# Kernel tuning notes

Measured on AMD Instinct MI355X. Metric: run time of the kernel, lower is better.

## Reference

```python
import jax, jax.numpy as jnp
import numpy as np

B, N, D = 128, 196, 1024          # batch, num image features, d_model == hidden_dim
E = 1024                           # embed_dim
V = 10000                          # vocab_size
NH = 8                             # num_heads
T = 20                             # max caption length
DH = D // NH


def setup_inputs() -> dict:
    key = jax.random.key(0)
    ks = jax.random.split(key, 16)
    u = lambda k, shape, s=0.1: jax.random.uniform(k, shape, jnp.float32, -s, s)
    lengths = jnp.sort(jax.random.randint(ks[1], (B,), 1, T + 1))[::-1]
    lengths = lengths.at[0].set(T)  # ensure max(lengths) == T
    return {
        "enc_features": jax.random.normal(ks[0], (B, N, D), jnp.float32),
        "captions": jax.random.randint(ks[2], (B, T), 0, V),
        "lengths": lengths,
        "embed_W": u(ks[3], (V, E)),
        # LSTMCell params (PyTorch layout: gates ordered i,f,g,o)
        "W_ih": u(ks[4], (4 * D, E + D), 0.03),
        "b_ih": u(ks[5], (4 * D,), 0.03),
        "W_hh": u(ks[6], (4 * D, D), 0.03),
        "b_hh": u(ks[7], (4 * D,), 0.03),
        # AoA block
        "Wq": u(ks[8], (D, D), 0.03), "bq": jnp.zeros((D,), jnp.float32),
        "Wk": u(ks[9], (D, D), 0.03), "bk": jnp.zeros((D,), jnp.float32),
        "Wv": u(ks[10], (D, D), 0.03), "bv": jnp.zeros((D,), jnp.float32),
        "W_aoa": u(ks[11], (2 * D, 2 * D), 0.02), "b_aoa": jnp.zeros((2 * D,), jnp.float32),
        # weight-normed predict layer (dim=0): W = g * v / ||v||_row
        "pred_v": u(ks[12], (V, D)),
        "pred_g": jnp.ones((V,), jnp.float32),
        "pred_b": jnp.zeros((V,), jnp.float32),
    }


def reference(enc_features, captions, lengths, embed_W, W_ih, b_ih, W_hh, b_hh,
              Wq, bq, Wk, bk, Wv, bv, W_aoa, b_aoa, pred_v, pred_g, pred_b):
    # eval mode: dropouts are identity; ss_prob == 0.
    scale = 1.0 / jnp.sqrt(jnp.asarray(DH, jnp.float32))
    mean_f = jnp.mean(enc_features, axis=1)                      # [B, D]
    # K/V projections of enc_features are step-invariant: hoist out of the loop.
    K = (enc_features @ Wk.T + bk).reshape(B, N, NH, DH).transpose(0, 2, 1, 3)  # [B,NH,N,DH]
    Vv = (enc_features @ Wv.T + bv).reshape(B, N, NH, DH).transpose(0, 2, 1, 3)
    # weight-norm predict matrix (dim=0 row-wise norm)
    Wn = pred_g[:, None] * pred_v / jnp.linalg.norm(pred_v, axis=1, keepdims=True)  # [V, D]

    active = (jnp.arange(T)[:, None] < lengths[None, :])         # [T, B]
    toks = captions.T                                            # [T, B]

    def step(carry, inp):
        h, m, ctx = carry
        it, act = inp
        emb = embed_W[it]                                        # [B, E]
        x = jnp.concatenate([emb, mean_f + ctx], axis=-1)        # [B, E+D]
        gates = x @ W_ih.T + b_ih + h @ W_hh.T + b_hh            # [B, 4D]
        i, f, g, o = jnp.split(gates, 4, axis=-1)
        m2 = jax.nn.sigmoid(f) * m + jax.nn.sigmoid(i) * jnp.tanh(g)
        h2 = jax.nn.sigmoid(o) * jnp.tanh(m2)                    # [B, D]
        # single-query multi-head attention
        q = (h2 @ Wq.T + bq).reshape(B, NH, DH)                  # [B, NH, DH]
        scores = jnp.einsum('bhd,bhnd->bhn', q, K) * scale       # [B, NH, N]
        p = jax.nn.softmax(scores, axis=-1)
        att = jnp.einsum('bhn,bhnd->bhd', p, Vv).reshape(B, D)   # [B, D]
        # AoA: Linear(2D->2D) + GLU on cat(att, query)
        a = jnp.concatenate([att, h2], axis=-1) @ W_aoa.T + b_aoa
        a1, a2 = jnp.split(a, 2, axis=-1)
        ctx2 = a1 * jax.nn.sigmoid(a2)                           # [B, D]
        preds = ctx2 @ Wn.T + pred_b                             # [B, V]
        preds = jnp.where(act[:, None], preds, 0.0)
        return (h2, m2, ctx2), preds

    z = jnp.zeros((B, D), jnp.float32)
    _, preds = jax.lax.scan(step, (z, z, z), (toks, active))     # [T, B, V]
    return preds.transpose(1, 0, 2)                              # [B, T, V], zero-padded
```

## Files before the change

### kernel.cpp

```cpp
#include <hip/hip_runtime.h>
#include <hip/hip_bf16.h>
#include <cstdint>

#define BB 128
#define TT 20
#define VV 10000
#define DD 1024
#define NHH 8
#define DHH 128
#define NN 196

typedef float f32x4 __attribute__((ext_vector_type(4)));
typedef __bf16 bf16x8 __attribute__((ext_vector_type(8)));
typedef unsigned int u32x4 __attribute__((ext_vector_type(4)));
typedef unsigned int u32x2 __attribute__((ext_vector_type(2)));

__device__ __forceinline__ unsigned short f2bf(float x) {
  unsigned u = __float_as_uint(x);
  u += 0x7FFFu + ((u >> 16) & 1u);
  return (unsigned short)(u >> 16);
}
__device__ __forceinline__ float bf2f(unsigned short h) {
  return __uint_as_float(((unsigned)h) << 16);
}
__device__ __forceinline__ float sigm(float x) { return 1.f / (1.f + __expf(-x)); }
__device__ __forceinline__ unsigned pk2(float lo, float hi) {
  return (unsigned)f2bf(lo) | ((unsigned)f2bf(hi) << 16);
}
__device__ __forceinline__ int xcd_swz(int orig, int nb) {
  int q = nb >> 3, r = nb & 7;
  int x = orig & 7, i = orig >> 3;
  return (x < r ? x * (q + 1) : r * (q + 1) + (x - r) * q) + i;
}
__device__ __forceinline__ void gl16(const void* g, void* l) {
  __builtin_amdgcn_global_load_lds((const __attribute__((address_space(1))) void*)g,
                                   (__attribute__((address_space(3))) void*)l, 16, 0, 0);
}

template<int N> __device__ __forceinline__ void waitvm() {
  if constexpr (N == 0)       asm volatile("s_waitcnt vmcnt(0)" ::: "memory");
  else if constexpr (N == 3)  asm volatile("s_waitcnt vmcnt(3)" ::: "memory");
  else if constexpr (N == 5)  asm volatile("s_waitcnt vmcnt(5)" ::: "memory");
  else if constexpr (N == 6)  asm volatile("s_waitcnt vmcnt(6)" ::: "memory");
  else if constexpr (N == 8)  asm volatile("s_waitcnt vmcnt(8)" ::: "memory");
  else if constexpr (N == 10) asm volatile("s_waitcnt vmcnt(10)" ::: "memory");
  else if constexpr (N == 12) asm volatile("s_waitcnt vmcnt(12)" ::: "memory");
  else if constexpr (N == 16) asm volatile("s_waitcnt vmcnt(16)" ::: "memory");
}
#define LGKM0()  asm volatile("s_waitcnt lgkmcnt(0)" ::: "memory")
#define SCHED0() __builtin_amdgcn_sched_barrier(0)

template<int BM, int BN, int MODE, int DEP, bool RF>
__launch_bounds__(256)
__global__ void gemmp(const unsigned short* __restrict__ A, int lda,
                      const unsigned short* __restrict__ W, int ldw,
                      int nkt, int N, int ncol,
                      const float* __restrict__ bias,
                      float* __restrict__ outF, unsigned short* __restrict__ outB,
                      float* __restrict__ mbuf, const float* __restrict__ meanf,
                      unsigned short* __restrict__ xaoa, unsigned short* __restrict__ xn2,
                      const int* __restrict__ lengths)
{
  constexpr int SZA = BM * 128;
  constexpr int SZB = BN * 128;
  constexpr int NJ = BN / 16;
  constexpr int MI = BM / 64;
  constexpr int S = BM / 32 + BN / 32;
  __shared__ char smem[DEP * (SZA + SZB)];

  const int nb = gridDim.x;
  const int wg = xcd_swz(blockIdx.x, nb);
  int xi, rowt;
  if (RF) { const int nrow = nb / ncol; rowt = wg % nrow; xi = wg / nrow; }
  else    { xi = wg % ncol; rowt = wg / ncol; }
  const int colbase = xi * BN;
  const int rowbase = rowt * BM;
  const int tid = threadIdx.x;
  const int lane = tid & 63, wv = tid >> 6;
  const int wrow = wv * (BM / 4);
  const int lr = lane & 15;
  const int srow = lane >> 3;
  const int schunk = ((lane & 7) ^ srow) * 8;

  auto stage = [&](int t, int buf) {
    char* sA = smem + buf * (SZA + SZB);
    char* sB = sA + SZA;
    const int k0 = t << 6;
    #pragma unroll
    for (int s = 0; s < BM / 32; ++s) {
      const int rb = s * 32 + wv * 8;
      gl16(A + (size_t)(rowbase + rb + srow) * lda + k0 + schunk, sA + rb * 128);
    }
    #pragma unroll
    for (int s = 0; s < BN / 32; ++s) {
      const int rb = s * 32 + wv * 8;
      int br = colbase + rb + srow;
      if (MODE == 2) br = br < N ? br : N - 1;
      gl16(W + (size_t)br * ldw + k0 + schunk, sB + rb * 128);
    }
  };

  f32x4 acc[MI][NJ];
  const f32x4 zero = {0.f, 0.f, 0.f, 0.f};
  #pragma unroll
  for (int i = 0; i < MI; ++i)
    #pragma unroll
    for (int j = 0; j < NJ; ++j) acc[i][j] = zero;

  #pragma unroll
  for (int t = 0; t < DEP; ++t) stage(t, t);

  const int axor = (lr & 7) << 4;
  const int ccol = (lane >> 4) * 16;
  int buf = 0;
  for (int i = 0; i < nkt; ++i) {
    const int rem = nkt - 1 - i;
    if (rem >= DEP - 1)            waitvm<S * (DEP - 1)>();
    else if (DEP > 2 && rem == 1)  waitvm<S>();
    else                           waitvm<0>();
    __builtin_amdgcn_s_barrier();
    SCHED0();
    const char* sA = smem + buf * (SZA + SZB);
    const char* sB = sA + SZA;
    bf16x8 af[MI][2], bfr[NJ][2];
    #pragma unroll
    for (int ii = 0; ii < MI; ++ii)
      #pragma unroll
      for (int kk = 0; kk < 2; ++kk)
        af[ii][kk] = *reinterpret_cast<const bf16x8*>(
            sA + (wrow + ii * 16 + lr) * 128 + ((kk * 64 + ccol) ^ axor));
    #pragma unroll
    for (int j = 0; j < NJ; ++j)
      #pragma unroll
      for (int kk = 0; kk < 2; ++kk)
        bfr[j][kk] = *reinterpret_cast<const bf16x8*>(
            sB + (j * 16 + lr) * 128 + ((kk * 64 + ccol) ^ axor));
    LGKM0();
    SCHED0();
    __builtin_amdgcn_s_barrier();
    SCHED0();
    if (i + DEP < nkt) stage(i + DEP, buf);
    #pragma unroll
    for (int kk = 0; kk < 2; ++kk)
      #pragma unroll
      for (int ii = 0; ii < MI; ++ii)
        #pragma unroll
        for (int j = 0; j < NJ; ++j)
          acc[ii][j] = __builtin_amdgcn_mfma_f32_16x16x32_bf16(af[ii][kk], bfr[j][kk], acc[ii][j], 0, 0, 0);
    buf = (buf == DEP - 1) ? 0 : buf + 1;
  }

  const int rg4 = (lane >> 4) * 4;

  if constexpr (MODE == 0) {
    #pragma unroll
    for (int ii = 0; ii < MI; ++ii)
      #pragma unroll
      for (int j = 0; j < NJ; ++j) {
        const int gcol = colbase + j * 16 + lr;
        #pragma unroll
        for (int r = 0; r < 4; ++r)
          outF[(size_t)(rowbase + wrow + ii * 16 + rg4 + r) * N + gcol] = acc[ii][j][r];
      }
  } else if constexpr (MODE == 1) {
    #pragma unroll
    for (int ii = 0; ii < MI; ++ii)
      #pragma unroll
      for (int j = 0; j < NJ; ++j) {
        const int gcol = colbase + j * 16 + lr;
        const float bv = bias[gcol];
        #pragma unroll
        for (int r = 0; r < 4; ++r)
          outB[(size_t)(rowbase + wrow + ii * 16 + rg4 + r) * N + gcol] = f2bf(acc[ii][j][r] + bv);
      }
  } else if constexpr (MODE == 2) {
    #pragma unroll
    for (int ii = 0; ii < MI; ++ii)
      #pragma unroll
      for (int j = 0; j < NJ; ++j) {
        const int gcol = colbase + j * 16 + lr;
        if (gcol >= N) continue;
        const float bv = bias[gcol];
        #pragma unroll
        for (int r = 0; r < 4; ++r) {
          const int gr = rowbase + wrow + ii * 16 + rg4 + r;
          const int tt = gr >> 7, bb = gr & 127;
          outF[((size_t)bb * TT + tt) * VV + gcol] =
              (tt < lengths[bb]) ? acc[ii][j][r] + bv : 0.f;
        }
      }
  } else if constexpr (MODE == 3) {
    const float b0 = bias[colbase + lr], b1 = bias[colbase + 16 + lr];
    float a0[MI][4], a1[MI][4];
    #pragma unroll
    for (int ii = 0; ii < MI; ++ii)
      #pragma unroll
      for (int r = 0; r < 4; ++r) {
        const int grow = rowbase + wrow + ii * 16 + rg4 + r;
        a0[ii][r] = acc[ii][0][r] + b0 + outF[(size_t)grow * 4096 + colbase + lr];
        a1[ii][r] = acc[ii][1][r] + b1 + outF[(size_t)grow * 4096 + colbase + 16 + lr];
      }
    const int d = (colbase >> 2) + (lr & 7);
    #pragma unroll
    for (int ii = 0; ii < MI; ++ii)
      #pragma unroll
      for (int r = 0; r < 4; ++r) {
        const float fg = __shfl_xor(a0[ii][r], 8);
        const float og = __shfl_xor(a1[ii][r], 8);
        if (lr < 8) {
          const int grow = rowbase + wrow + ii * 16 + rg4 + r;
          const float m2 = sigm(fg) * mbuf[(size_t)grow * DD + d] + sigm(a0[ii][r]) * tanhf(a1[ii][r]);
          const float h2 = sigm(og) * tanhf(m2);
          mbuf[(size_t)grow * DD + d] = m2;
          const unsigned short hb = f2bf(h2);
          xaoa[(size_t)grow * 2048 + 1024 + d] = hb;
          xn2[(size_t)grow * 2048 + 1024 + d] = hb;
        }
      }
  } else {
    const int d = (colbase >> 1) + lr;
    const float b0 = bias[colbase + lr], b1 = bias[colbase + 16 + lr];
    #pragma unroll
    for (int ii = 0; ii < MI; ++ii)
      #pragma unroll
      for (int r = 0; r < 4; ++r) {
        const int grow = rowbase + wrow + ii * 16 + rg4 + r;
        const float av1 = acc[ii][0][r] + b0;
        const float av2 = acc[ii][1][r] + b1;
        const float c2 = av1 * sigm(av2);
        outB[(size_t)grow * DD + d] = f2bf(c2);
        xn2[(size_t)grow * 2048 + d] = f2bf(meanf[(size_t)grow * DD + d] + c2);
      }
  }
}

__launch_bounds__(256)
__global__ void attn_kernel(const float* __restrict__ qbuf, const float* __restrict__ bq,
                            const unsigned short* __restrict__ KV, unsigned short* __restrict__ xaoa) {
  const int bh = blockIdx.x, b = bh >> 3, h = bh & 7;
  const int tid = threadIdx.x;
  const int lane = tid & 63, wv = tid >> 6;
  __shared__ float qs[DHH];
  __shared__ float sc[NN + 4];
  __shared__ float pvred[2][DHH];
  __shared__ float redm[4], reds[4];
  if (tid < DHH)
    qs[tid] = bq[h * DHH + tid] + qbuf[(size_t)b * DD + h * DHH + tid];
  __syncthreads();
  if (tid < NN) {
    const unsigned short* kr = KV + ((size_t)(b * NN + tid)) * 2048 + h * DHH;
    float a = 0.f;
    #pragma unroll
    for (int j = 0; j < 16; ++j) {
      u32x4 kk = *reinterpret_cast<const u32x4*>(kr + j * 8);
      #pragma unroll
      for (int w = 0; w < 4; ++w) {
        a += bf2f((unsigned short)(kk[w] & 0xffffu)) * qs[j * 8 + w * 2]
           + bf2f((unsigned short)(kk[w] >> 16)) * qs[j * 8 + w * 2 + 1];
      }
    }
    sc[tid] = a * 0.08838834764831845f;
  }
  __syncthreads();
  float v = (tid < NN) ? sc[tid] : -1e30f;
  #pragma unroll
  for (int o = 32; o; o >>= 1) v = fmaxf(v, __shfl_xor(v, o));
  if (lane == 0) redm[wv] = v;
  __syncthreads();
  const float mx = fmaxf(fmaxf(redm[0], redm[1]), fmaxf(redm[2], redm[3]));
  float e = 0.f;
  if (tid < NN) { e = __expf(sc[tid] - mx); sc[tid] = e; }
  float s = e;
  #pragma unroll
  for (int o = 32; o; o >>= 1) s += __shfl_xor(s, o);
  if (lane == 0) reds[wv] = s;
  __syncthreads();
  const float inv = 1.f / (reds[0] + reds[1] + reds[2] + reds[3]);
  const int d = tid & 127, half = tid >> 7;
  const unsigned short* vr = KV + ((size_t)(b * NN + half * 98)) * 2048 + 1024 + h * DHH + d;
  float a = 0.f;
  for (int n = 0; n < 98; ++n) a += sc[half * 98 + n] * bf2f(vr[(size_t)n * 2048]);
  pvred[half][d] = a;
  __syncthreads();
  if (tid < DHH)
    xaoa[(size_t)b * 2048 + h * DHH + tid] = f2bf((pvred[0][tid] + pvred[1][tid]) * inv);
}

__launch_bounds__(256)
__global__ void meanconv_kernel(const float* __restrict__ enc, float* __restrict__ meanf,
                                unsigned short* __restrict__ encb) {
  int b = blockIdx.x >> 2, d = (blockIdx.x & 3) * 256 + threadIdx.x;
  const float* p = enc + (size_t)b * NN * DD + d;
  unsigned short* q = encb + (size_t)b * NN * DD + d;
  float s = 0.f;
  for (int n = 0; n < NN; ++n) {
    float x = p[(size_t)n * DD];
    s += x;
    q[(size_t)n * DD] = f2bf(x);
  }
  meanf[(size_t)b * DD + d] = s * (1.0f / (float)NN);
}

__launch_bounds__(256)
__global__ void conv4_kernel(const float* __restrict__ src, unsigned short* __restrict__ dst) {
  int i = blockIdx.x * 256 + threadIdx.x;
  f32x4 v = *reinterpret_cast<const f32x4*>(src + (size_t)i * 4);
  u32x2 o = { pk2(v[0], v[1]), pk2(v[2], v[3]) };
  *reinterpret_cast<u32x2*>(dst + (size_t)i * 4) = o;
}

__launch_bounds__(256)
__global__ void wcatI_kernel(const float* __restrict__ W_ih, const float* __restrict__ W_hh,
                             unsigned short* __restrict__ Wcat) {
  int i = blockIdx.x * 256 + threadIdx.x;
  int rp = i / 768, c4 = (i - rp * 768) * 4;
  int rem = rp & 31, g = rem >> 3, d = (rp >> 5) * 8 + (rem & 7);
  int orig = g * 1024 + d;
  const float* src = (c4 < 2048) ? (W_ih + (size_t)orig * 2048 + c4)
                                 : (W_hh + (size_t)orig * 1024 + (c4 - 2048));
  f32x4 v = *reinterpret_cast<const f32x4*>(src);
  u32x2 o = { pk2(v[0], v[1]), pk2(v[2], v[3]) };
  *reinterpret_cast<u32x2*>(Wcat + (size_t)rp * 3072 + c4) = o;
}

__launch_bounds__(256)
__global__ void waoaI_kernel(const float* __restrict__ W_aoa, unsigned short* __restrict__ Wo) {
  int i = blockIdx.x * 256 + threadIdx.x;
  int rp = i >> 9, c4 = (i & 511) * 4;
  int rem = rp & 31, half = rem >> 4, d = (rp >> 5) * 16 + (rem & 15);
  int orig = half * 1024 + d;
  f32x4 v = *reinterpret_cast<const f32x4*>(W_aoa + (size_t)orig * 2048 + c4);
  u32x2 o = { pk2(v[0], v[1]), pk2(v[2], v[3]) };
  *reinterpret_cast<u32x2*>(Wo + (size_t)rp * 2048 + c4) = o;
}

__launch_bounds__(256)
__global__ void kvw4_kernel(const float* __restrict__ Wk, const float* __restrict__ Wv,
                            unsigned short* __restrict__ Wkv) {
  int i = blockIdx.x * 256 + threadIdx.x;
  int row = i >> 8, c4 = (i & 255) << 2;
  const float* src = (row < 1024) ? (Wk + (size_t)row * 1024 + c4)
                                  : (Wv + (size_t)(row - 1024) * 1024 + c4);
  f32x4 v = *reinterpret_cast<const f32x4*>(src);
  u32x2 o = { pk2(v[0], v[1]), pk2(v[2], v[3]) };
  *reinterpret_cast<u32x2*>(Wkv + (size_t)row * 1024 + c4) = o;
}

__launch_bounds__(256)
__global__ void bias_kernel(const float* __restrict__ b_ih, const float* __restrict__ b_hh,
                            const float* __restrict__ b_aoa, const float* __restrict__ bk,
                            const float* __restrict__ bv, float* __restrict__ bcombI,
                            float* __restrict__ baoaI, float* __restrict__ bkv) {
  int i = blockIdx.x * 256 + threadIdx.x;
  {
    int rem = i & 31, g = rem >> 3, d = (i >> 5) * 8 + (rem & 7);
    int orig = g * 1024 + d;
    bcombI[i] = b_ih[orig] + b_hh[orig];
  }
  if (i < 2048) {
    int rem = i & 31, half = rem >> 4, d = (i >> 5) * 16 + (rem & 15);
    baoaI[i] = b_aoa[half * 1024 + d];
    bkv[i] = (i < 1024) ? bk[i] : bv[i - 1024];
  }
}

__launch_bounds__(256)
__global__ void init_kernel(const float* __restrict__ meanf, float* __restrict__ m,
                            unsigned short* __restrict__ x2_0) {
  int idx = blockIdx.x * 256 + threadIdx.x;
  int b = idx >> 10, d = idx & 1023;
  m[idx] = 0.f;
  x2_0[(size_t)b * 2048 + d] = f2bf(meanf[idx]);
  x2_0[(size_t)b * 2048 + 1024 + d] = 0;
}

__launch_bounds__(256)
__global__ void wn_kernel(const float* __restrict__ pred_v, const float* __restrict__ pred_g,
                          unsigned short* __restrict__ Wn) {
  int v = blockIdx.x, tid = threadIdx.x;
  f32x4 x = *reinterpret_cast<const f32x4*>(pred_v + (size_t)v * DD + tid * 4);
  float s = x[0] * x[0] + x[1] * x[1] + x[2] * x[2] + x[3] * x[3];
  #pragma unroll
  for (int o = 32; o; o >>= 1) s += __shfl_down(s, o);
  __shared__ float red[4];
  if ((tid & 63) == 0) red[tid >> 6] = s;
  __syncthreads();
  float inv = pred_g[v] * rsqrtf(red[0] + red[1] + red[2] + red[3]);
  u32x2 o = { pk2(x[0] * inv, x[1] * inv), pk2(x[2] * inv, x[3] * inv) };
  *reinterpret_cast<u32x2*>(Wn + (size_t)v * DD + tid * 4) = o;
}

__launch_bounds__(256)
__global__ void emb4_kernel(const float* __restrict__ embed_W, const int* __restrict__ captions,
                            unsigned short* __restrict__ embAll) {
  int i = blockIdx.x * 256 + threadIdx.x;
  int j4 = (i & 255) << 2, b = (i >> 8) & 127, t = i >> 15;
  int tok = captions[b * TT + t];
  f32x4 v = *reinterpret_cast<const f32x4*>(embed_W + (size_t)tok * DD + j4);
  u32x2 o = { pk2(v[0], v[1]), pk2(v[2], v[3]) };
  *reinterpret_cast<u32x2*>(embAll + ((size_t)t * BB + b) * DD + j4) = o;
}

extern "C" void kernel_launch(void* const* d_in, const int* in_sizes, int n_in,
                              void* d_out, int out_size, void* d_ws, size_t ws_size,
                              hipStream_t stream) {
  const float* enc      = (const float*)d_in[0];
  const int*   captions = (const int*)d_in[1];
  const int*   lengths  = (const int*)d_in[2];
  const float* embed_W  = (const float*)d_in[3];
  const float* W_ih     = (const float*)d_in[4];
  const float* b_ih     = (const float*)d_in[5];
  const float* W_hh     = (const float*)d_in[6];
  const float* b_hh     = (const float*)d_in[7];
  const float* Wq       = (const float*)d_in[8];
  const float* bq       = (const float*)d_in[9];
  const float* Wk       = (const float*)d_in[10];
  const float* bk       = (const float*)d_in[11];
  const float* Wv       = (const float*)d_in[12];
  const float* bv       = (const float*)d_in[13];
  const float* W_aoa    = (const float*)d_in[14];
  const float* b_aoa    = (const float*)d_in[15];
  const float* pred_v   = (const float*)d_in[16];
  const float* pred_g   = (const float*)d_in[17];
  const float* pred_b   = (const float*)d_in[18];
  float* out = (float*)d_out;

  char* base = (char*)d_ws;
  size_t off = 0;
  auto alloc = [&](size_t bytes) -> char* {
    char* p = base + off;
    off = (off + bytes + 255) & ~(size_t)255;
    return p;
  };
  unsigned short* KV     = (unsigned short*)alloc((size_t)BB * NN * 2048 * 2);
  unsigned short* WcatI  = (unsigned short*)alloc((size_t)4096 * 3072 * 2);
  unsigned short* WaoaI  = (unsigned short*)alloc((size_t)2048 * 2048 * 2);
  unsigned short* Wq_b   = (unsigned short*)alloc((size_t)DD * DD * 2);
  unsigned short* Wkv_b  = (unsigned short*)alloc((size_t)2048 * 1024 * 2);
  float* bcombI          = (float*)alloc(4096 * 4);
  float* baoaI           = (float*)alloc(2048 * 4);
  float* bkv             = (float*)alloc(2048 * 4);
  float* meanf           = (float*)alloc((size_t)BB * DD * 4);
  float* mbuf            = (float*)alloc((size_t)BB * DD * 4);
  unsigned short* embAll = (unsigned short*)alloc((size_t)TT * BB * DD * 2);
  unsigned short* x2     = (unsigned short*)alloc((size_t)2 * BB * 2048 * 2);
  char* uni = alloc((size_t)BB * NN * DD * 2);
  unsigned short* encb = (unsigned short*)uni;
  size_t ua = 0;
  auto carve = [&](size_t b) -> char* { char* p = uni + ua; ua = (ua + b + 255) & ~(size_t)255; return p; };
  float* Eall               = (float*)carve((size_t)TT * BB * 4096 * 4);
  unsigned short* predinAll = (unsigned short*)carve((size_t)TT * BB * DD * 2);
  unsigned short* xaoa      = (unsigned short*)carve((size_t)BB * 2048 * 2);
  float* qbuf               = (float*)carve((size_t)BB * DD * 4);
  unsigned short* Wn_b      = (unsigned short*)uni;
  if (off > ws_size || ua > (size_t)BB * NN * DD * 2) return;

  meanconv_kernel<<<512, 256, 0, stream>>>(enc, meanf, encb);
  wcatI_kernel<<<12288, 256, 0, stream>>>(W_ih, W_hh, WcatI);
  conv4_kernel<<<1024, 256, 0, stream>>>(Wq, Wq_b);
  waoaI_kernel<<<4096, 256, 0, stream>>>(W_aoa, WaoaI);
  kvw4_kernel<<<2048, 256, 0, stream>>>(Wk, Wv, Wkv_b);
  bias_kernel<<<16, 256, 0, stream>>>(b_ih, b_hh, b_aoa, bk, bv, bcombI, baoaI, bkv);
  emb4_kernel<<<2560, 256, 0, stream>>>(embed_W, captions, embAll);
  init_kernel<<<512, 256, 0, stream>>>(meanf, mbuf, x2);
  gemmp<128, 128, 1, 2, false><<<3136, 256, 0, stream>>>(encb, 1024, Wkv_b, 1024, 16, 2048, 16, bkv,
                                                         nullptr, KV, nullptr, nullptr, nullptr, nullptr, nullptr);
  gemmp<128, 128, 0, 2, true><<<640, 256, 0, stream>>>(embAll, 1024, WcatI, 3072, 16, 4096, 32, nullptr,
                                                       Eall, nullptr, nullptr, nullptr, nullptr, nullptr, nullptr);

  for (int t = 0; t < TT; ++t) {
    unsigned short* xc = x2 + (size_t)(t & 1) * BB * 2048;
    unsigned short* xn = x2 + (size_t)((t + 1) & 1) * BB * 2048;
    gemmp<64, 32, 3, 3, false><<<256, 256, 0, stream>>>(xc, 2048, WcatI + 1024, 3072, 32, 4096, 128, bcombI,
                                                        Eall + (size_t)t * BB * 4096, nullptr, mbuf, nullptr, xaoa, xn, nullptr);
    gemmp<64, 32, 0, 3, false><<<64, 256, 0, stream>>>(xaoa + 1024, 2048, Wq_b, 1024, 16, 1024, 32, nullptr,
                                                       qbuf, nullptr, nullptr, nullptr, nullptr, nullptr, nullptr);
    attn_kernel<<<BB * NHH, 256, 0, stream>>>(qbuf, bq, KV, xaoa);
    gemmp<64, 32, 4, 3, false><<<128, 256, 0, stream>>>(xaoa, 2048, WaoaI, 2048, 32, 2048, 64, baoaI,
                                                        nullptr, predinAll + (size_t)t * BB * DD, nullptr, meanf, nullptr, xn, nullptr);
  }

  wn_kernel<<<VV, 256, 0, stream>>>(pred_v, pred_g, Wn_b);
  gemmp<128, 128, 2, 2, true><<<1580, 256, 0, stream>>>(predinAll, 1024, Wn_b, 1024, 16, VV, 79, pred_b,
                                                        out, nullptr, nullptr, nullptr, nullptr, nullptr, lengths);
}
```

Measured before the change: 1.269 ms.

## Merge prep kernels into one launch, halve GEMM M-tile, split PV accumulators

Seven small preprocessing kernels (weight conversions, biases, embedding gather, init) are merged into one prep_kernel that dispatches on block index, removing per-launch overhead. The KV projection and final prediction GEMMs switch from 128x128 to 64x128 tiles with twice the grid, aiming for better CU occupancy and load balance. The attention PV loop uses two accumulators with partial unrolling to expose more memory-level parallelism. Smaller tiles reduce data reuse per block, and the block-index branching adds some divergence risk.

```diff
diff --git a/kernel.cpp b/kernel.cpp
--- a/kernel.cpp
+++ b/kernel.cpp
@@ -278,12 +278,93 @@
   const float inv = 1.f / (reds[0] + reds[1] + reds[2] + reds[3]);
   const int d = tid & 127, half = tid >> 7;
   const unsigned short* vr = KV + ((size_t)(b * NN + half * 98)) * 2048 + 1024 + h * DHH + d;
-  float a = 0.f;
-  for (int n = 0; n < 98; ++n) a += sc[half * 98 + n] * bf2f(vr[(size_t)n * 2048]);
-  pvred[half][d] = a;
+  const float* pr = sc + half * 98;
+  float a0 = 0.f, a1 = 0.f;
+  #pragma unroll 7
+  for (int n = 0; n < 98; n += 2) {
+    a0 += pr[n]     * bf2f(vr[(size_t)n * 2048]);
+    a1 += pr[n + 1] * bf2f(vr[(size_t)(n + 1) * 2048]);
+  }
+  pvred[half][d] = a0 + a1;
   __syncthreads();
   if (tid < DHH)
     xaoa[(size_t)b * 2048 + h * DHH + tid] = f2bf((pvred[0][tid] + pvred[1][tid]) * inv);
+}
+
+__launch_bounds__(256)
+__global__ void prep_kernel(const float* __restrict__ W_ih, const float* __restrict__ W_hh,
+                            const float* __restrict__ Wq, const float* __restrict__ W_aoa,
+                            const float* __restrict__ Wk, const float* __restrict__ Wv,
+                            const float* __restrict__ b_ih, const float* __restrict__ b_hh,
+                            const float* __restrict__ b_aoa, const float* __restrict__ bk,
+                            const float* __restrict__ bv,
+                            const float* __restrict__ embed_W, const int* __restrict__ captions,
+                            const float* __restrict__ meanf,
+                            unsigned short* __restrict__ WcatI, unsigned short* __restrict__ Wq_b,
+                            unsigned short* __restrict__ WaoaI, unsigned short* __restrict__ Wkv_b,
+                            float* __restrict__ bcombI, float* __restrict__ baoaI,
+                            float* __restrict__ bkv,
+                            unsigned short* __restrict__ embAll, float* __restrict__ mbuf,
+                            unsigned short* __restrict__ x2_0)
+{
+  const int bid = blockIdx.x, tid = threadIdx.x;
+  if (bid < 12288) {
+    int i = bid * 256 + tid;
+    int rp = i / 768, c4 = (i - rp * 768) * 4;
+    int rem = rp & 31, g = rem >> 3, d = (rp >> 5) * 8 + (rem & 7);
+    int orig = g * 1024 + d;
+    const float* src = (c4 < 2048) ? (W_ih + (size_t)orig * 2048 + c4)
+                                   : (W_hh + (size_t)orig * 1024 + (c4 - 2048));
+    f32x4 vv = *reinterpret_cast<const f32x4*>(src);
+    u32x2 o = { pk2(vv[0], vv[1]), pk2(vv[2], vv[3]) };
+    *reinterpret_cast<u32x2*>(WcatI + (size_t)rp * 3072 + c4) = o;
+  } else if (bid < 13312) {
+    int i = (bid - 12288) * 256 + tid;
+    f32x4 vv = *reinterpret_cast<const f32x4*>(Wq + (size_t)i * 4);
+    u32x2 o = { pk2(vv[0], vv[1]), pk2(vv[2], vv[3]) };
+    *reinterpret_cast<u32x2*>(Wq_b + (size_t)i * 4) = o;
+  } else if (bid < 17408) {
+    int i = (bid - 13312) * 256 + tid;
+    int rp = i >> 9, c4 = (i & 511) * 4;
+    int rem = rp & 31, half = rem >> 4, d = (rp >> 5) * 16 + (rem & 15);
+    int orig = half * 1024 + d;
+    f32x4 vv = *reinterpret_cast<const f32x4*>(W_aoa + (size_t)orig * 2048 + c4);
+    u32x2 o = { pk2(vv[0], vv[1]), pk2(vv[2], vv[3]) };
+    *reinterpret_cast<u32x2*>(WaoaI + (size_t)rp * 2048 + c4) = o;
+  } else if (bid < 19456) {
+    int i = (bid - 17408) * 256 + tid;
+    int row = i >> 8, c4 = (i & 255) << 2;
+    const float* src = (row < 1024) ? (Wk + (size_t)row * 1024 + c4)
+                                    : (Wv + (size_t)(row - 1024) * 1024 + c4);
+    f32x4 vv = *reinterpret_cast<const f32x4*>(src);
+    u32x2 o = { pk2(vv[0], vv[1]), pk2(vv[2], vv[3]) };
+    *reinterpret_cast<u32x2*>(Wkv_b + (size_t)row * 1024 + c4) = o;
+  } else if (bid < 19472) {
+    int i = (bid - 19456) * 256 + tid;
+    {
+      int rem = i & 31, g = rem >> 3, d = (i >> 5) * 8 + (rem & 7);
+      int orig = g * 1024 + d;
+      bcombI[i] = b_ih[orig] + b_hh[orig];
+    }
+    if (i < 2048) {
+      int rem = i & 31, half = rem >> 4, d = (i >> 5) * 16 + (rem & 15);
+      baoaI[i] = b_aoa[half * 1024 + d];
+      bkv[i] = (i < 1024) ? bk[i] : bv[i - 1024];
+    }
+  } else if (bid < 22032) {
+    int i = (bid - 19472) * 256 + tid;
+    int j4 = (i & 255) << 2, b = (i >> 8) & 127, t = i >> 15;
+    int tok = captions[b * TT + t];
+    f32x4 vv = *reinterpret_cast<const f32x4*>(embed_W + (size_t)tok * DD + j4);
+    u32x2 o = { pk2(vv[0], vv[1]), pk2(vv[2], vv[3]) };
+    *reinterpret_cast<u32x2*>(embAll + ((size_t)t * BB + b) * DD + j4) = o;
+  } else {
+    int idx = (bid - 22032) * 256 + tid;
+    int b = idx >> 10, d = idx & 1023;
+    mbuf[idx] = 0.f;
+    x2_0[(size_t)b * 2048 + d] = f2bf(meanf[idx]);
+    x2_0[(size_t)b * 2048 + 1024 + d] = 0;
+  }
 }
 
 __launch_bounds__(256)
@@ -302,79 +383,6 @@
 }
 
 __launch_bounds__(256)
-__global__ void conv4_kernel(const float* __restrict__ src, unsigned short* __restrict__ dst) {
-  int i = blockIdx.x * 256 + threadIdx.x;
-  f32x4 v = *reinterpret_cast<const f32x4*>(src + (size_t)i * 4);
-  u32x2 o = { pk2(v[0], v[1]), pk2(v[2], v[3]) };
-  *reinterpret_cast<u32x2*>(dst + (size_t)i * 4) = o;
-}
-
-__launch_bounds__(256)
-__global__ void wcatI_kernel(const float* __restrict__ W_ih, const float* __restrict__ W_hh,
-                             unsigned short* __restrict__ Wcat) {
-  int i = blockIdx.x * 256 + threadIdx.x;
-  int rp = i / 768, c4 = (i - rp * 768) * 4;
-  int rem = rp & 31, g = rem >> 3, d = (rp >> 5) * 8 + (rem & 7);
-  int orig = g * 1024 + d;
-  const float* src = (c4 < 2048) ? (W_ih + (size_t)orig * 2048 + c4)
-                                 : (W_hh + (size_t)orig * 1024 + (c4 - 2048));
-  f32x4 v = *reinterpret_cast<const f32x4*>(src);
-  u32x2 o = { pk2(v[0], v[1]), pk2(v[2], v[3]) };
-  *reinterpret_cast<u32x2*>(Wcat + (size_t)rp * 3072 + c4) = o;
-}
-
-__launch_bounds__(256)
-__global__ void waoaI_kernel(const float* __restrict__ W_aoa, unsigned short* __restrict__ Wo) {
-  int i = blockIdx.x * 256 + threadIdx.x;
-  int rp = i >> 9, c4 = (i & 511) * 4;
-  int rem = rp & 31, half = rem >> 4, d = (rp >> 5) * 16 + (rem & 15);
-  int orig = half * 1024 + d;
-  f32x4 v = *reinterpret_cast<const f32x4*>(W_aoa + (size_t)orig * 2048 + c4);
-  u32x2 o = { pk2(v[0], v[1]), pk2(v[2], v[3]) };
-  *reinterpret_cast<u32x2*>(Wo + (size_t)rp * 2048 + c4) = o;
-}
-
-__launch_bounds__(256)
-__global__ void kvw4_kernel(const float* __restrict__ Wk, const float* __restrict__ Wv,
-                            unsigned short* __restrict__ Wkv) {
-  int i = blockIdx.x * 256 + threadIdx.x;
-  int row = i >> 8, c4 = (i & 255) << 2;
-  const float* src = (row < 1024) ? (Wk + (size_t)row * 1024 + c4)
-                                  : (Wv + (size_t)(row - 1024) * 1024 + c4);
-  f32x4 v = *reinterpret_cast<const f32x4*>(src);
-  u32x2 o = { pk2(v[0], v[1]), pk2(v[2], v[3]) };
-  *reinterpret_cast<u32x2*>(Wkv + (size_t)row * 1024 + c4) = o;
-}
-
-__launch_bounds__(256)
-__global__ void bias_kernel(const float* __restrict__ b_ih, const float* __restrict__ b_hh,
-                            const float* __restrict__ b_aoa, const float* __restrict__ bk,
-                            const float* __restrict__ bv, float* __restrict__ bcombI,
-                            float* __restrict__ baoaI, float* __restrict__ bkv) {
-  int i = blockIdx.x * 256 + threadIdx.x;
-  {
-    int rem = i & 31, g = rem >> 3, d = (i >> 5) * 8 + (rem & 7);
-    int orig = g * 1024 + d;
-    bcombI[i] = b_ih[orig] + b_hh[orig];
-  }
-  if (i < 2048) {
-    int rem = i & 31, half = rem >> 4, d = (i >> 5) * 16 + (rem & 15);
-    baoaI[i] = b_aoa[half * 1024 + d];
-    bkv[i] = (i < 1024) ? bk[i] : bv[i - 1024];
-  }
-}
-
-__launch_bounds__(256)
-__global__ void init_kernel(const float* __restrict__ meanf, float* __restrict__ m,
-                            unsigned short* __restrict__ x2_0) {
-  int idx = blockIdx.x * 256 + threadIdx.x;
-  int b = idx >> 10, d = idx & 1023;
-  m[idx] = 0.f;
-  x2_0[(size_t)b * 2048 + d] = f2bf(meanf[idx]);
-  x2_0[(size_t)b * 2048 + 1024 + d] = 0;
-}
-
-__launch_bounds__(256)
 __global__ void wn_kernel(const float* __restrict__ pred_v, const float* __restrict__ pred_g,
                           unsigned short* __restrict__ Wn) {
   int v = blockIdx.x, tid = threadIdx.x;
@@ -388,17 +396,6 @@
   float inv = pred_g[v] * rsqrtf(red[0] + red[1] + red[2] + red[3]);
   u32x2 o = { pk2(x[0] * inv, x[1] * inv), pk2(x[2] * inv, x[3] * inv) };
   *reinterpret_cast<u32x2*>(Wn + (size_t)v * DD + tid * 4) = o;
-}
-
-__launch_bounds__(256)
-__global__ void emb4_kernel(const float* __restrict__ embed_W, const int* __restrict__ captions,
-                            unsigned short* __restrict__ embAll) {
-  int i = blockIdx.x * 256 + threadIdx.x;
-  int j4 = (i & 255) << 2, b = (i >> 8) & 127, t = i >> 15;
-  int tok = captions[b * TT + t];
-  f32x4 v = *reinterpret_cast<const f32x4*>(embed_W + (size_t)tok * DD + j4);
-  u32x2 o = { pk2(v[0], v[1]), pk2(v[2], v[3]) };
-  *reinterpret_cast<u32x2*>(embAll + ((size_t)t * BB + b) * DD + j4) = o;
 }
 
 extern "C" void kernel_launch(void* const* d_in, const int* in_sizes, int n_in,
@@ -456,15 +453,13 @@
   if (off > ws_size || ua > (size_t)BB * NN * DD * 2) return;
 
   meanconv_kernel<<<512, 256, 0, stream>>>(enc, meanf, encb);
-  wcatI_kernel<<<12288, 256, 0, stream>>>(W_ih, W_hh, WcatI);
-  conv4_kernel<<<1024, 256, 0, stream>>>(Wq, Wq_b);
-  waoaI_kernel<<<4096, 256, 0, stream>>>(W_aoa, WaoaI);
-  kvw4_kernel<<<2048, 256, 0, stream>>>(Wk, Wv, Wkv_b);
-  bias_kernel<<<16, 256, 0, stream>>>(b_ih, b_hh, b_aoa, bk, bv, bcombI, baoaI, bkv);
-  emb4_kernel<<<2560, 256, 0, stream>>>(embed_W, captions, embAll);
-  init_kernel<<<512, 256, 0, stream>>>(meanf, mbuf, x2);
-  gemmp<128, 128, 1, 2, false><<<3136, 256, 0, stream>>>(encb, 1024, Wkv_b, 1024, 16, 2048, 16, bkv,
-                                                         nullptr, KV, nullptr, nullptr, nullptr, nullptr, nullptr);
+  prep_kernel<<<22544, 256, 0, stream>>>(W_ih, W_hh, Wq, W_aoa, Wk, Wv,
+                                         b_ih, b_hh, b_aoa, bk, bv,
+                                         embed_W, captions, meanf,
+                                         WcatI, Wq_b, WaoaI, Wkv_b,
+                                         bcombI, baoaI, bkv, embAll, mbuf, x2);
+  gemmp<64, 128, 1, 2, false><<<6272, 256, 0, stream>>>(encb, 1024, Wkv_b, 1024, 16, 2048, 16, bkv,
+                                                        nullptr, KV, nullptr, nullptr, nullptr, nullptr, nullptr);
   gemmp<128, 128, 0, 2, true><<<640, 256, 0, stream>>>(embAll, 1024, WcatI, 3072, 16, 4096, 32, nullptr,
                                                        Eall, nullptr, nullptr, nullptr, nullptr, nullptr, nullptr);
 
@@ -481,6 +476,6 @@
   }
 
   wn_kernel<<<VV, 256, 0, stream>>>(pred_v, pred_g, Wn_b);
-  gemmp<128, 128, 2, 2, true><<<1580, 256, 0, stream>>>(predinAll, 1024, Wn_b, 1024, 16, VV, 79, pred_b,
-                                                        out, nullptr, nullptr, nullptr, nullptr, nullptr, lengths);
-}
+  gemmp<64, 128, 2, 2, true><<<3160, 256, 0, stream>>>(predinAll, 1024, Wn_b, 1024, 16, VV, 79, pred_b,
+                                                       out, nullptr, nullptr, nullptr, nullptr, nullptr, lengths);
+}
```

After: 1.299 ms. 1.02x slower.
